# Kernel optimization log

Measured on AMD Instinct MI355X. Metric: run time of the kernel, lower is better.

The kernel has to match this reference:

```python
import jax, jax.numpy as jnp
import numpy as np

N_EMBED = 384
T_MAX = 256
EPS = 1e-5


def layer_norm(x, gamma, beta):
    mu = jnp.mean(x, axis=-1, keepdims=True)
    var = jnp.mean(jnp.square(x - mu), axis=-1, keepdims=True)
    return (x - mu) * jax.lax.rsqrt(var + EPS) * gamma + beta


def setup_inputs() -> dict:
    key = jax.random.key(0)
    ks = jax.random.split(key, 12)
    B, T, C = 128, 256, N_EMBED
    s = lambda fan_in: 1.0 / np.sqrt(fan_in)
    return {
        "x": jax.random.normal(ks[0], (B, T, C), dtype=jnp.float32),
        "W_attn": jax.random.uniform(ks[1], (C, 3 * C), minval=-s(C), maxval=s(C), dtype=jnp.float32),
        "b_attn": jax.random.uniform(ks[2], (3 * C,), minval=-s(C), maxval=s(C), dtype=jnp.float32),
        "W_proj": jax.random.uniform(ks[3], (C, C), minval=-s(C), maxval=s(C), dtype=jnp.float32),
        "b_proj": jax.random.uniform(ks[4], (C,), minval=-s(C), maxval=s(C), dtype=jnp.float32),
        "ln1_g": jnp.ones((C,), jnp.float32),
        "ln1_b": jnp.zeros((C,), jnp.float32),
        "ln2_g": jnp.ones((C,), jnp.float32),
        "ln2_b": jnp.zeros((C,), jnp.float32),
        "W1": jax.random.uniform(ks[5], (C, 4 * C), minval=-s(C), maxval=s(C), dtype=jnp.float32),
        "b1": jax.random.uniform(ks[6], (4 * C,), minval=-s(C), maxval=s(C), dtype=jnp.float32),
        "W2": jax.random.uniform(ks[7], (4 * C, C), minval=-s(4 * C), maxval=s(4 * C), dtype=jnp.float32),
        "b2": jax.random.uniform(ks[8], (4 * C,)[:1] and (C,), minval=-s(4 * C), maxval=s(4 * C), dtype=jnp.float32),
    }


def reference(x, W_attn, b_attn, W_proj, b_proj, ln1_g, ln1_b, ln2_g, ln2_b, W1, b1, W2, b2):
    B, T, C = x.shape
    # --- pre-LN single-head causal self-attention ---
    h = layer_norm(x, ln1_g, ln1_b)
    qkv = h @ W_attn + b_attn                      # [B,T,3C]
    q, k, v = jnp.split(qkv, 3, axis=-1)           # each [B,T,C]
    att = jnp.einsum('btc,bsc->bts', q, k) * (1.0 / jnp.sqrt(jnp.float32(C)))
    causal = jnp.tril(jnp.ones((T, T), bool))
    att = jnp.where(causal, att, -jnp.inf)
    att = jax.nn.softmax(att, axis=-1)             # dropout is identity (eval)
    y = jnp.einsum('bts,bsc->btc', att, v)
    x = x + (y @ W_proj + b_proj)
    # --- pre-LN MLP ---
    h2 = layer_norm(x, ln2_g, ln2_b)
    x = x + (jax.nn.relu(h2 @ W1 + b1) @ W2 + b2)
    return x
```

## Files before the change

### kernel.cpp

```cpp
#include <hip/hip_runtime.h>
#include <hip/hip_bf16.h>

#define C_EMB 384
#define T_SEQ 256
#define B_BATCH 128
#define M_ROWS (B_BATCH * T_SEQ)
#define QKV_LD 1152
#define BK 64

typedef __bf16 bf16_8 __attribute__((ext_vector_type(8)));
typedef float f32x4 __attribute__((ext_vector_type(4)));

__device__ __forceinline__ void load16_lds(const __bf16* g, __bf16* l) {
    __builtin_amdgcn_global_load_lds(
        (const __attribute__((address_space(1))) unsigned int*)g,
        (__attribute__((address_space(3))) unsigned int*)l, 16, 0, 0);
}

__global__ __launch_bounds__(256) void cast_all_kernel(const float* __restrict__ Wa,
                                                       const float* __restrict__ Wp,
                                                       const float* __restrict__ W1,
                                                       const float* __restrict__ W2,
                                                       __bf16* __restrict__ Wa_t,
                                                       __bf16* __restrict__ Wp_t,
                                                       __bf16* __restrict__ W1_t,
                                                       __bf16* __restrict__ W2_t) {
    int bid = blockIdx.x;
    const float* W; __bf16* Wt; int K, N, tx_n;
    if (bid < 432)      { W = Wa; Wt = Wa_t; K = 384;  N = 1152; tx_n = 36; }
    else if (bid < 576) { bid -= 432; W = Wp; Wt = Wp_t; K = 384;  N = 384;  tx_n = 12; }
    else if (bid < 1152){ bid -= 576; W = W1; Wt = W1_t; K = 384;  N = 1536; tx_n = 48; }
    else                { bid -= 1152; W = W2; Wt = W2_t; K = 1536; N = 384;  tx_n = 12; }
    int n0 = (bid % tx_n) * 32, k0 = (bid / tx_n) * 32;

    __shared__ float t[32][33];
    int tx = threadIdx.x & 31, ty = threadIdx.x >> 5;
#pragma unroll
    for (int i = 0; i < 4; ++i)
        t[ty + i * 8][tx] = W[(size_t)(k0 + ty + i * 8) * N + n0 + tx];
    __syncthreads();
#pragma unroll
    for (int i = 0; i < 4; ++i) {
        int n = ty + i * 8;
        Wt[(size_t)(n0 + n) * K + k0 + tx] = (__bf16)t[tx][n];
    }
}

__global__ __launch_bounds__(384) void ln_kernel(const float* __restrict__ x,
                                                 const float* __restrict__ g,
                                                 const float* __restrict__ bta,
                                                 __bf16* __restrict__ out) {
    int row = blockIdx.x;
    int c = threadIdx.x;
    float v = x[(size_t)row * C_EMB + c];

    __shared__ float red[6];
    float s = v;
#pragma unroll
    for (int o = 32; o; o >>= 1) s += __shfl_down(s, o);
    if ((c & 63) == 0) red[c >> 6] = s;
    __syncthreads();
    float mu = (red[0] + red[1] + red[2] + red[3] + red[4] + red[5]) * (1.0f / C_EMB);

    float d = v - mu;
    float s2 = d * d;
#pragma unroll
    for (int o = 32; o; o >>= 1) s2 += __shfl_down(s2, o);
    __syncthreads();
    if ((c & 63) == 0) red[c >> 6] = s2;
    __syncthreads();
    float var = (red[0] + red[1] + red[2] + red[3] + red[4] + red[5]) * (1.0f / C_EMB);

    out[(size_t)row * C_EMB + c] = (__bf16)(d * rsqrtf(var + 1e-5f) * g[c] + bta[c]);
}

template <int TM, bool RELU, bool RESID, bool OUT_BF16>
__global__ __launch_bounds__(256) void mfma_gemm(const __bf16* __restrict__ A, int lda,
                                                 const __bf16* __restrict__ Bt, int ldb,
                                                 const float* __restrict__ bias,
                                                 const float* __restrict__ resid,
                                                 void* __restrict__ out_,
                                                 int N, int K) {
    constexpr int MI = TM / 32;
    constexpr int WROWS = TM / 2;
    __shared__ __align__(16) __bf16 As[2 * TM * 32];
    __shared__ __align__(16) __bf16 Bs[2 * 128 * 32];

    int tid = threadIdx.x;
    int wave = tid >> 6, lane = tid & 63;
    int wr = wave >> 1, wc = wave & 1;
    int quad = lane >> 4, l16 = lane & 15;
    int bm = blockIdx.y * TM, bn = blockIdx.x * 128;
    int lrow = lane >> 2, lcol = (lane & 3) * 8;

    f32x4 acc[MI][4] = {};

    for (int k0 = 0; k0 < K; k0 += BK) {
        const __bf16* Ab = A + (size_t)bm * lda + k0;
        const __bf16* Bb = Bt + (size_t)bn * ldb + k0;
#pragma unroll
        for (int p = 0; p < 2; ++p) {
#pragma unroll
            for (int i = 0; i < TM / 64; ++i) {
                int r0 = (i * 4 + wave) * 16;
                load16_lds(Ab + (size_t)(r0 + lrow) * lda + p * 32 + lcol,
                           &As[p * TM * 32 + r0 * 32]);
            }
#pragma unroll
            for (int i = 0; i < 2; ++i) {
                int r0 = (i * 4 + wave) * 16;
                load16_lds(Bb + (size_t)(r0 + lrow) * ldb + p * 32 + lcol,
                           &Bs[p * 128 * 32 + r0 * 32]);
            }
        }
        __syncthreads();

        bf16_8 af[MI][2], bf[4][2];
#pragma unroll
        for (int p = 0; p < 2; ++p) {
#pragma unroll
            for (int i = 0; i < MI; ++i)
                af[i][p] = *reinterpret_cast<const bf16_8*>(
                    &As[p * TM * 32 + (wr * WROWS + i * 16 + l16) * 32 + quad * 8]);
#pragma unroll
            for (int j = 0; j < 4; ++j)
                bf[j][p] = *reinterpret_cast<const bf16_8*>(
                    &Bs[p * 128 * 32 + (wc * 64 + j * 16 + l16) * 32 + quad * 8]);
        }
#pragma unroll
        for (int i = 0; i < MI; ++i)
#pragma unroll
            for (int j = 0; j < 4; ++j) {
                acc[i][j] = __builtin_amdgcn_mfma_f32_16x16x32_bf16(af[i][0], bf[j][0], acc[i][j], 0, 0, 0);
                acc[i][j] = __builtin_amdgcn_mfma_f32_16x16x32_bf16(af[i][1], bf[j][1], acc[i][j], 0, 0, 0);
            }
        __syncthreads();
    }

#pragma unroll
    for (int i = 0; i < MI; ++i) {
#pragma unroll
        for (int r = 0; r < 4; ++r) {
            int m = bm + wr * WROWS + i * 16 + quad * 4 + r;
#pragma unroll
            for (int j = 0; j < 4; ++j) {
                int n = bn + wc * 64 + j * 16 + l16;
                float v = acc[i][j][r] + bias[n];
                if (RELU) v = fmaxf(v, 0.0f);
                if (RESID) v += resid[(size_t)m * N + n];
                if (OUT_BF16)
                    ((__bf16*)out_)[(size_t)m * N + n] = (__bf16)v;
                else
                    ((float*)out_)[(size_t)m * N + n] = v;
            }
        }
    }
}

__global__ __launch_bounds__(512, 1) void ff2_kernel(const __bf16* __restrict__ A,
                                                     const __bf16* __restrict__ Bt,
                                                     const float* __restrict__ bias,
                                                     float* __restrict__ out) {
    __shared__ __align__(16) __bf16 At[2][128 * 64];
    __shared__ __align__(16) __bf16 Bs[2][384 * 64];

    int tid = threadIdx.x;
    int wave = tid >> 6, lane = tid & 63;
    int wr = wave >> 1, wc = wave & 1;
    int quad = lane >> 4, l16 = lane & 15;
    int bm = blockIdx.x * 128;
    int srow = lane >> 3;
    int sunit = (lane & 7) ^ srow;

    const __bf16* asrc0 = A + (size_t)(bm + srow) * 1536 + sunit * 8;
    const __bf16* bsrc0 = Bt + (size_t)srow * 1536 + sunit * 8;

    auto stage = [&](int buf, int k0) {
#pragma unroll
        for (int t = 0; t < 2; ++t) {
            int g = t * 8 + wave;
            load16_lds(asrc0 + (size_t)(g * 8) * 1536 + k0, &At[buf][g * 8 * 64]);
        }
#pragma unroll
        for (int t = 0; t < 6; ++t) {
            int g = t * 8 + wave;
            load16_lds(bsrc0 + (size_t)(g * 8) * 1536 + k0, &Bs[buf][g * 8 * 64]);
        }
    };

    f32x4 acc[2][12] = {};

    stage(0, 0);
    asm volatile("s_waitcnt vmcnt(0)" ::: "memory");
    __builtin_amdgcn_sched_barrier(0);
    __builtin_amdgcn_s_barrier();

#pragma unroll 2
    for (int kt = 0; kt < 24; ++kt) {
        int cur = kt & 1;
        if (kt < 23) stage(cur ^ 1, (kt + 1) * BK);

        bf16_8 af[2][2];
#pragma unroll
        for (int p = 0; p < 2; ++p)
#pragma unroll
            for (int i = 0; i < 2; ++i) {
                int row = wr * 32 + i * 16 + l16;
                int u = (p * 4 + quad) ^ (row & 7);
                af[i][p] = *reinterpret_cast<const bf16_8*>(&At[cur][row * 64 + u * 8]);
            }
#pragma unroll
        for (int p = 0; p < 2; ++p)
#pragma unroll
            for (int j = 0; j < 12; ++j) {
                int row = wc * 192 + j * 16 + l16;
                int u = (p * 4 + quad) ^ (row & 7);
                bf16_8 bf = *reinterpret_cast<const bf16_8*>(&Bs[cur][row * 64 + u * 8]);
                acc[0][j] = __builtin_amdgcn_mfma_f32_16x16x32_bf16(af[0][p], bf, acc[0][j], 0, 0, 0);
                acc[1][j] = __builtin_amdgcn_mfma_f32_16x16x32_bf16(af[1][p], bf, acc[1][j], 0, 0, 0);
            }

        asm volatile("s_waitcnt vmcnt(0)" ::: "memory");
        __builtin_amdgcn_sched_barrier(0);
        __builtin_amdgcn_s_barrier();
    }

#pragma unroll
    for (int i = 0; i < 2; ++i)
#pragma unroll
        for (int r = 0; r < 4; ++r) {
            int m = bm + wr * 32 + i * 16 + quad * 4 + r;
#pragma unroll
            for (int j = 0; j < 12; ++j) {
                int n = wc * 192 + j * 16 + l16;
                float* o = &out[(size_t)m * C_EMB + n];
                *o = *o + acc[i][j][r] + bias[n];
            }
        }
}

__global__ __launch_bounds__(256) void proj_ln_kernel(const __bf16* __restrict__ A,
                                                      const __bf16* __restrict__ Bt,
                                                      const float* __restrict__ bias,
                                                      const float* __restrict__ resid,
                                                      const float* __restrict__ lng,
                                                      const float* __restrict__ lnb,
                                                      float* __restrict__ out,
                                                      __bf16* __restrict__ h) {
    __shared__ __align__(16) __bf16 As[2 * 64 * 32];
    __shared__ __align__(16) __bf16 Bs[2 * 384 * 32];
    __shared__ float red[2][2][64];

    int tid = threadIdx.x;
    int wave = tid >> 6, lane = tid & 63;
    int wr = wave >> 1, wc = wave & 1;
    int quad = lane >> 4, l16 = lane & 15;
    int bm = blockIdx.x * 64;
    int lrow = lane >> 2, lcol = (lane & 3) * 8;

    f32x4 acc[2][12] = {};

    for (int k0 = 0; k0 < C_EMB; k0 += BK) {
        const __bf16* Ab = A + (size_t)bm * C_EMB + k0;
        const __bf16* Bb = Bt + k0;
#pragma unroll
        for (int p = 0; p < 2; ++p) {
            {
                int r0 = wave * 16;
                load16_lds(Ab + (size_t)(r0 + lrow) * C_EMB + p * 32 + lcol,
                           &As[p * 64 * 32 + r0 * 32]);
            }
#pragma unroll
            for (int i = 0; i < 6; ++i) {
                int r0 = (i * 4 + wave) * 16;
                load16_lds(Bb + (size_t)(r0 + lrow) * C_EMB + p * 32 + lcol,
                           &Bs[p * 384 * 32 + r0 * 32]);
            }
        }
        __syncthreads();

        bf16_8 af[2][2], bf[12][2];
#pragma unroll
        for (int p = 0; p < 2; ++p) {
#pragma unroll
            for (int i = 0; i < 2; ++i)
                af[i][p] = *reinterpret_cast<const bf16_8*>(
                    &As[p * 64 * 32 + (wr * 32 + i * 16 + l16) * 32 + quad * 8]);
#pragma unroll
            for (int j = 0; j < 12; ++j)
                bf[j][p] = *reinterpret_cast<const bf16_8*>(
                    &Bs[p * 384 * 32 + (wc * 192 + j * 16 + l16) * 32 + quad * 8]);
        }
#pragma unroll
        for (int i = 0; i < 2; ++i)
#pragma unroll
            for (int j = 0; j < 12; ++j) {
                acc[i][j] = __builtin_amdgcn_mfma_f32_16x16x32_bf16(af[i][0], bf[j][0], acc[i][j], 0, 0, 0);
                acc[i][j] = __builtin_amdgcn_mfma_f32_16x16x32_bf16(af[i][1], bf[j][1], acc[i][j], 0, 0, 0);
            }
        __syncthreads();
    }

    float bia[12], gg[12], bb[12];
#pragma unroll
    for (int j = 0; j < 12; ++j) {
        int n = wc * 192 + j * 16 + l16;
        bia[j] = bias[n];
        gg[j] = lng[n];
        bb[j] = lnb[n];
    }

#pragma unroll
    for (int i = 0; i < 2; ++i)
#pragma unroll
        for (int r = 0; r < 4; ++r) {
            int rloc = wr * 32 + i * 16 + quad * 4 + r;
            int m = bm + rloc;
            float s = 0.0f, s2 = 0.0f;
#pragma unroll
            for (int j = 0; j < 12; ++j) {
                int n = wc * 192 + j * 16 + l16;
                float v = acc[i][j][r] + bia[j] + resid[(size_t)m * C_EMB + n];
                acc[i][j][r] = v;
                s += v;
                s2 += v * v;
            }
#pragma unroll
            for (int o = 8; o; o >>= 1) {
                s += __shfl_xor(s, o);
                s2 += __shfl_xor(s2, o);
            }
            if (l16 == 0) {
                red[0][wc][rloc] = s;
                red[1][wc][rloc] = s2;
            }
        }
    __syncthreads();

#pragma unroll
    for (int i = 0; i < 2; ++i)
#pragma unroll
        for (int r = 0; r < 4; ++r) {
            int rloc = wr * 32 + i * 16 + quad * 4 + r;
            int m = bm + rloc;
            float mu  = (red[0][0][rloc] + red[0][1][rloc]) * (1.0f / C_EMB);
            float ex2 = (red[1][0][rloc] + red[1][1][rloc]) * (1.0f / C_EMB);
            float rstd = rsqrtf(ex2 - mu * mu + 1e-5f);
#pragma unroll
            for (int j = 0; j < 12; ++j) {
                int n = wc * 192 + j * 16 + l16;
                float v = acc[i][j][r];
                out[(size_t)m * C_EMB + n] = v;
                h[(size_t)m * C_EMB + n] = (__bf16)((v - mu) * rstd * gg[j] + bb[j]);
            }
        }
}

__global__ __launch_bounds__(256) void vt_kernel(const __bf16* __restrict__ qkv,
                                                 __bf16* __restrict__ Vt) {
    __shared__ __align__(16) __bf16 t[32][72];
    int b = blockIdx.z, c0 = blockIdx.x * 64, s0 = blockIdx.y * 32;
    int tid = threadIdx.x;

    int tx = tid & 7, ty = tid >> 3;
    const __bf16* src = qkv + ((size_t)b * T_SEQ + s0 + ty) * QKV_LD + 768 + c0 + tx * 8;
    *reinterpret_cast<float4*>(&t[ty][tx * 8]) = *reinterpret_cast<const float4*>(src);
    __syncthreads();

    int sx = tid & 3, cy = tid >> 2;
    __align__(16) __bf16 tmp[8];
#pragma unroll
    for (int j = 0; j < 8; ++j) tmp[j] = t[sx * 8 + j][cy];
    *reinterpret_cast<float4*>(&Vt[((size_t)b * C_EMB + c0 + cy) * T_SEQ + s0 + sx * 8]) =
        *reinterpret_cast<float4*>(tmp);
}

__global__ __launch_bounds__(256) void qks_mfma(const __bf16* __restrict__ qkv,
                                                __bf16* __restrict__ P) {
    int b = blockIdx.y;
    int bx = blockIdx.x;
    int bm = bx * 128;
    int ntiles = bx + 1;
    const __bf16* Ab0 = qkv + (size_t)b * T_SEQ * QKV_LD;
    const __bf16* Bb0 = Ab0 + 384;

    __shared__ __align__(16) __bf16 As[2 * 128 * 32];
    __shared__ __align__(16) __bf16 Bs[2 * 128 * 32];
    __shared__ float red[2][2][128];

    int tid = threadIdx.x;
    int wave = tid >> 6, lane = tid & 63;
    int wr = wave >> 1, wc = wave & 1;
    int quad = lane >> 4, l16 = lane & 15;
    int lrow = lane >> 2, lcol = (lane & 3) * 8;

    f32x4 acc[2][4][4] = {};

#pragma unroll
    for (int nt = 0; nt < 2; ++nt) {
        if (nt < ntiles) {
            int bn = nt * 128;
            for (int k0 = 0; k0 < C_EMB; k0 += BK) {
                const __bf16* Ab = Ab0 + (size_t)bm * QKV_LD + k0;
                const __bf16* Bb = Bb0 + (size_t)bn * QKV_LD + k0;
#pragma unroll
                for (int p = 0; p < 2; ++p)
#pragma unroll
                    for (int i = 0; i < 2; ++i) {
                        int r0 = (i * 4 + wave) * 16;
                        load16_lds(Ab + (size_t)(r0 + lrow) * QKV_LD + p * 32 + lcol,
                                   &As[p * 128 * 32 + r0 * 32]);
                        load16_lds(Bb + (size_t)(r0 + lrow) * QKV_LD + p * 32 + lcol,
                                   &Bs[p * 128 * 32 + r0 * 32]);
                    }
                __syncthreads();

                bf16_8 af[4][2], bf[4][2];
#pragma unroll
                for (int p = 0; p < 2; ++p)
#pragma unroll
                    for (int i = 0; i < 4; ++i) {
                        af[i][p] = *reinterpret_cast<const bf16_8*>(
                            &As[p * 128 * 32 + (wr * 64 + i * 16 + l16) * 32 + quad * 8]);
                        bf[i][p] = *reinterpret_cast<const bf16_8*>(
                            &Bs[p * 128 * 32 + (wc * 64 + i * 16 + l16) * 32 + quad * 8]);
                    }
#pragma unroll
                for (int i = 0; i < 4; ++i)
#pragma unroll
                    for (int j = 0; j < 4; ++j) {
                        acc[nt][i][j] = __builtin_amdgcn_mfma_f32_16x16x32_bf16(af[i][0], bf[j][0], acc[nt][i][j], 0, 0, 0);
                        acc[nt][i][j] = __builtin_amdgcn_mfma_f32_16x16x32_bf16(af[i][1], bf[j][1], acc[nt][i][j], 0, 0, 0);
                    }
                __syncthreads();
            }
        }
    }

    const float scale = 0.05103103630798288f;

#pragma unroll
    for (int i = 0; i < 4; ++i)
#pragma unroll
        for (int r = 0; r < 4; ++r) {
            int rloc = wr * 64 + i * 16 + quad * 4 + r;
            int t = bm + rloc;
            float m = -INFINITY;
#pragma unroll
            for (int nt = 0; nt < 2; ++nt)
#pragma unroll
                for (int j = 0; j < 4; ++j) {
                    int n = nt * 128 + wc * 64 + j * 16 + l16;
                    bool ok = (nt < ntiles) && (n <= t);
                    float v = acc[nt][i][j][r] * scale;
                    m = fmaxf(m, ok ? v : -INFINITY);
                }
#pragma unroll
            for (int o = 8; o; o >>= 1) m = fmaxf(m, __shfl_xor(m, o));
            if (l16 == 0) red[0][wc][rloc] = m;
        }
    __syncthreads();

#pragma unroll
    for (int i = 0; i < 4; ++i)
#pragma unroll
        for (int r = 0; r < 4; ++r) {
            int rloc = wr * 64 + i * 16 + quad * 4 + r;
            int t = bm + rloc;
            float M = fmaxf(red[0][0][rloc], red[0][1][rloc]);
            float s = 0.0f;
#pragma unroll
            for (int nt = 0; nt < 2; ++nt)
#pragma unroll
                for (int j = 0; j < 4; ++j) {
                    int n = nt * 128 + wc * 64 + j * 16 + l16;
                    bool ok = (nt < ntiles) && (n <= t);
                    float p = ok ? __expf(acc[nt][i][j][r] * scale - M) : 0.0f;
                    acc[nt][i][j][r] = p;
                    s += p;
                }
#pragma unroll
            for (int o = 8; o; o >>= 1) s += __shfl_xor(s, o);
            if (l16 == 0) red[1][wc][rloc] = s;
        }
    __syncthreads();

    __bf16* Pb_ = P + (size_t)b * T_SEQ * T_SEQ;
#pragma unroll
    for (int i = 0; i < 4; ++i)
#pragma unroll
        for (int r = 0; r < 4; ++r) {
            int rloc = wr * 64 + i * 16 + quad * 4 + r;
            float inv = 1.0f / (red[1][0][rloc] + red[1][1][rloc]);
#pragma unroll
            for (int nt = 0; nt < 2; ++nt)
                if (nt < ntiles)
#pragma unroll
                    for (int j = 0; j < 4; ++j) {
                        int n = nt * 128 + wc * 64 + j * 16 + l16;
                        Pb_[(size_t)(bm + rloc) * T_SEQ + n] = (__bf16)(acc[nt][i][j][r] * inv);
                    }
        }
}

__global__ __launch_bounds__(256) void pv_mfma(const __bf16* __restrict__ P,
                                               const __bf16* __restrict__ Vt,
                                               __bf16* __restrict__ y) {
    int b = blockIdx.z;
    int bm = blockIdx.y * 128, bn = blockIdx.x * 128;
    const __bf16* Ab0 = P + (size_t)b * T_SEQ * T_SEQ;
    const __bf16* Bb0 = Vt + (size_t)b * C_EMB * T_SEQ;

    __shared__ __align__(16) __bf16 As[2 * 128 * 32];
    __shared__ __align__(16) __bf16 Bs[2 * 128 * 32];

    int tid = threadIdx.x;
    int wave = tid >> 6, lane = tid & 63;
    int wr = wave >> 1, wc = wave & 1;
    int quad = lane >> 4, l16 = lane & 15;
    int lrow = lane >> 2, lcol = (lane & 3) * 8;

    f32x4 acc[4][4] = {};

    int kmax = bm + 128;
    for (int k0 = 0; k0 < kmax; k0 += BK) {
        const __bf16* Ab = Ab0 + (size_t)bm * T_SEQ + k0;
        const __bf16* Bb = Bb0 + (size_t)bn * T_SEQ + k0;
#pragma unroll
        for (int p = 0; p < 2; ++p)
#pragma unroll
            for (int i = 0; i < 2; ++i) {
                int r0 = (i * 4 + wave) * 16;
                load16_lds(Ab + (size_t)(r0 + lrow) * T_SEQ + p * 32 + lcol,
                           &As[p * 128 * 32 + r0 * 32]);
                load16_lds(Bb + (size_t)(r0 + lrow) * T_SEQ + p * 32 + lcol,
                           &Bs[p * 128 * 32 + r0 * 32]);
            }
        __syncthreads();

        bf16_8 af[4][2], bf[4][2];
#pragma unroll
        for (int p = 0; p < 2; ++p)
#pragma unroll
            for (int i = 0; i < 4; ++i) {
                af[i][p] = *reinterpret_cast<const bf16_8*>(
                    &As[p * 128 * 32 + (wr * 64 + i * 16 + l16) * 32 + quad * 8]);
                bf[i][p] = *reinterpret_cast<const bf16_8*>(
                    &Bs[p * 128 * 32 + (wc * 64 + i * 16 + l16) * 32 + quad * 8]);
            }
#pragma unroll
        for (int i = 0; i < 4; ++i)
#pragma unroll
            for (int j = 0; j < 4; ++j) {
                acc[i][j] = __builtin_amdgcn_mfma_f32_16x16x32_bf16(af[i][0], bf[j][0], acc[i][j], 0, 0, 0);
                acc[i][j] = __builtin_amdgcn_mfma_f32_16x16x32_bf16(af[i][1], bf[j][1], acc[i][j], 0, 0, 0);
            }
        __syncthreads();
    }

#pragma unroll
    for (int i = 0; i < 4; ++i) {
#pragma unroll
        for (int r = 0; r < 4; ++r) {
            int m = bm + wr * 64 + i * 16 + quad * 4 + r;
#pragma unroll
            for (int j = 0; j < 4; ++j) {
                int n = bn + wc * 64 + j * 16 + l16;
                y[((size_t)b * T_SEQ + m) * C_EMB + n] = (__bf16)acc[i][j][r];
            }
        }
    }
}

extern "C" void kernel_launch(void* const* d_in, const int* in_sizes, int n_in,
                              void* d_out, int out_size, void* d_ws, size_t ws_size,
                              hipStream_t stream) {
    const float* x      = (const float*)d_in[0];
    const float* W_attn = (const float*)d_in[1];
    const float* b_attn = (const float*)d_in[2];
    const float* W_proj = (const float*)d_in[3];
    const float* b_proj = (const float*)d_in[4];
    const float* ln1_g  = (const float*)d_in[5];
    const float* ln1_b  = (const float*)d_in[6];
    const float* ln2_g  = (const float*)d_in[7];
    const float* ln2_b  = (const float*)d_in[8];
    const float* W1     = (const float*)d_in[9];
    const float* b1     = (const float*)d_in[10];
    const float* W2     = (const float*)d_in[11];
    const float* b2     = (const float*)d_in[12];
    float* out = (float*)d_out;

    __bf16* Wattn_t = (__bf16*)d_ws;
    __bf16* Wproj_t = Wattn_t + (size_t)1152 * 384;
    __bf16* W1_t    = Wproj_t + (size_t)384 * 384;
    __bf16* W2_t    = W1_t + (size_t)1536 * 384;
    __bf16* h       = W2_t + (size_t)384 * 1536;
    __bf16* yb      = h + (size_t)M_ROWS * 384;
    __bf16* qkv     = yb + (size_t)M_ROWS * 384;
    float*  S       = (float*)(qkv + (size_t)M_ROWS * QKV_LD);
    __bf16* Pb      = (__bf16*)(S + (size_t)B_BATCH * T_SEQ * T_SEQ);
    __bf16* Vt      = Pb + (size_t)B_BATCH * T_SEQ * T_SEQ;
    __bf16* ff      = qkv;

    cast_all_kernel<<<1728, 256, 0, stream>>>(W_attn, W_proj, W1, W2,
                                              Wattn_t, Wproj_t, W1_t, W2_t);

    ln_kernel<<<M_ROWS, 384, 0, stream>>>(x, ln1_g, ln1_b, h);
    mfma_gemm<128, false, false, true><<<dim3(1152 / 128, M_ROWS / 128), 256, 0, stream>>>(
        h, 384, Wattn_t, 384, b_attn, nullptr, qkv, 1152, 384);
    vt_kernel<<<dim3(C_EMB / 64, T_SEQ / 32, B_BATCH), 256, 0, stream>>>(qkv, Vt);
    qks_mfma<<<dim3(2, B_BATCH), 256, 0, stream>>>(qkv, Pb);
    pv_mfma<<<dim3(C_EMB / 128, T_SEQ / 128, B_BATCH), 256, 0, stream>>>(Pb, Vt, yb);
    proj_ln_kernel<<<M_ROWS / 64, 256, 0, stream>>>(yb, Wproj_t, b_proj, x,
                                                    ln2_g, ln2_b, out, h);
    mfma_gemm<128, true, false, true><<<dim3(1536 / 128, M_ROWS / 128), 256, 0, stream>>>(
        h, 384, W1_t, 384, b1, nullptr, ff, 1536, 384);
    ff2_kernel<<<M_ROWS / 128, 512, 0, stream>>>(ff, W2_t, b2, out);
}
```

Baseline: 450.5 us.

## Shrink FF2 GEMM tile to 64 rows with BK=32 for higher occupancy

Reworks the second MLP GEMM kernel to use 64-row output tiles, a K step of 32 and a 2x4 wave layout, so LDS use drops from about 112KB to about 28KB per block. This allows up to four blocks per CU instead of one and doubles the grid to 512 blocks, which should improve latency hiding and load balance. In exchange each block reloads the full W2 tile for fewer rows, so weight traffic per output doubles, and the loop runs twice as many iterations with a barrier each.

Result: no change. 457.5 us (+1.6%).

```diff
diff --git a/kernel.cpp b/kernel.cpp
--- a/kernel.cpp
+++ b/kernel.cpp
@@ -157,38 +157,35 @@
     }
 }
 
-__global__ __launch_bounds__(512, 1) void ff2_kernel(const __bf16* __restrict__ A,
-                                                     const __bf16* __restrict__ Bt,
-                                                     const float* __restrict__ bias,
-                                                     float* __restrict__ out) {
-    __shared__ __align__(16) __bf16 At[2][128 * 64];
-    __shared__ __align__(16) __bf16 Bs[2][384 * 64];
+__global__ __launch_bounds__(512, 4) void ff2_pipe(const __bf16* __restrict__ A,
+                                                   const __bf16* __restrict__ Bt,
+                                                   const float* __restrict__ bias,
+                                                   float* __restrict__ out) {
+    __shared__ __align__(16) __bf16 At[2][64 * 32];
+    __shared__ __align__(16) __bf16 Bs[2][384 * 32];
 
     int tid = threadIdx.x;
     int wave = tid >> 6, lane = tid & 63;
-    int wr = wave >> 1, wc = wave & 1;
+    int wr = wave >> 2, wc = wave & 3;
     int quad = lane >> 4, l16 = lane & 15;
-    int bm = blockIdx.x * 128;
-    int srow = lane >> 3;
-    int sunit = (lane & 7) ^ srow;
+    int bm = blockIdx.x * 64;
+    int srow = lane >> 2;
+    int sunit = (lane & 3) ^ (srow & 3);
 
     const __bf16* asrc0 = A + (size_t)(bm + srow) * 1536 + sunit * 8;
     const __bf16* bsrc0 = Bt + (size_t)srow * 1536 + sunit * 8;
 
     auto stage = [&](int buf, int k0) {
-#pragma unroll
-        for (int t = 0; t < 2; ++t) {
+        if (wave < 4)
+            load16_lds(asrc0 + (size_t)(wave * 16) * 1536 + k0, &At[buf][wave * 16 * 32]);
+#pragma unroll
+        for (int t = 0; t < 3; ++t) {
             int g = t * 8 + wave;
-            load16_lds(asrc0 + (size_t)(g * 8) * 1536 + k0, &At[buf][g * 8 * 64]);
-        }
-#pragma unroll
-        for (int t = 0; t < 6; ++t) {
-            int g = t * 8 + wave;
-            load16_lds(bsrc0 + (size_t)(g * 8) * 1536 + k0, &Bs[buf][g * 8 * 64]);
+            load16_lds(bsrc0 + (size_t)(g * 16) * 1536 + k0, &Bs[buf][g * 16 * 32]);
         }
     };
 
-    f32x4 acc[2][12] = {};
+    f32x4 acc[2][6] = {};
 
     stage(0, 0);
     asm volatile("s_waitcnt vmcnt(0)" ::: "memory");
@@ -196,29 +193,25 @@
     __builtin_amdgcn_s_barrier();
 
 #pragma unroll 2
-    for (int kt = 0; kt < 24; ++kt) {
+    for (int kt = 0; kt < 48; ++kt) {
         int cur = kt & 1;
-        if (kt < 23) stage(cur ^ 1, (kt + 1) * BK);
-
-        bf16_8 af[2][2];
-#pragma unroll
-        for (int p = 0; p < 2; ++p)
-#pragma unroll
-            for (int i = 0; i < 2; ++i) {
-                int row = wr * 32 + i * 16 + l16;
-                int u = (p * 4 + quad) ^ (row & 7);
-                af[i][p] = *reinterpret_cast<const bf16_8*>(&At[cur][row * 64 + u * 8]);
-            }
-#pragma unroll
-        for (int p = 0; p < 2; ++p)
-#pragma unroll
-            for (int j = 0; j < 12; ++j) {
-                int row = wc * 192 + j * 16 + l16;
-                int u = (p * 4 + quad) ^ (row & 7);
-                bf16_8 bf = *reinterpret_cast<const bf16_8*>(&Bs[cur][row * 64 + u * 8]);
-                acc[0][j] = __builtin_amdgcn_mfma_f32_16x16x32_bf16(af[0][p], bf, acc[0][j], 0, 0, 0);
-                acc[1][j] = __builtin_amdgcn_mfma_f32_16x16x32_bf16(af[1][p], bf, acc[1][j], 0, 0, 0);
-            }
+        if (kt < 47) stage(cur ^ 1, (kt + 1) * 32);
+
+        bf16_8 af[2];
+#pragma unroll
+        for (int i = 0; i < 2; ++i) {
+            int row = wr * 32 + i * 16 + l16;
+            int u = quad ^ (row & 3);
+            af[i] = *reinterpret_cast<const bf16_8*>(&At[cur][row * 32 + u * 8]);
+        }
+#pragma unroll
+        for (int j = 0; j < 6; ++j) {
+            int row = wc * 96 + j * 16 + l16;
+            int u = quad ^ (row & 3);
+            bf16_8 bf = *reinterpret_cast<const bf16_8*>(&Bs[cur][row * 32 + u * 8]);
+            acc[0][j] = __builtin_amdgcn_mfma_f32_16x16x32_bf16(af[0], bf, acc[0][j], 0, 0, 0);
+            acc[1][j] = __builtin_amdgcn_mfma_f32_16x16x32_bf16(af[1], bf, acc[1][j], 0, 0, 0);
+        }
 
         asm volatile("s_waitcnt vmcnt(0)" ::: "memory");
         __builtin_amdgcn_sched_barrier(0);
@@ -231,8 +224,8 @@
         for (int r = 0; r < 4; ++r) {
             int m = bm + wr * 32 + i * 16 + quad * 4 + r;
 #pragma unroll
-            for (int j = 0; j < 12; ++j) {
-                int n = wc * 192 + j * 16 + l16;
+            for (int j = 0; j < 6; ++j) {
+                int n = wc * 96 + j * 16 + l16;
                 float* o = &out[(size_t)m * C_EMB + n];
                 *o = *o + acc[i][j][r] + bias[n];
             }
@@ -615,5 +608,5 @@
                                                     ln2_g, ln2_b, out, h);
     mfma_gemm<128, true, false, true><<<dim3(1536 / 128, M_ROWS / 128), 256, 0, stream>>>(
         h, 384, W1_t, 384, b1, nullptr, ff, 1536, 384);
-    ff2_kernel<<<M_ROWS / 128, 512, 0, stream>>>(ff, W2_t, b2, out);
-}
+    ff2_pipe<<<M_ROWS / 64, 512, 0, stream>>>(ff, W2_t, b2, out);
+}
```
